# Kernel optimization log

Measured on AMD Instinct MI355X. Metric: run time of the kernel, lower is better.

Reference implementation:

```python
import jax, jax.numpy as jnp
import numpy as np
from jax.scipy.linalg import expm

U_SHAPE = (4, 32, 16, 16, 16, 3, 3)   # [mu, t, x, y, z, 3, 3]
W_SHAPE = (8, 32, 16, 16, 16, 3, 3)   # [feature, t, x, y, z, 3, 3]


def setup_inputs() -> dict:
    key = jax.random.key(0)
    k = jax.random.split(key, 5)
    return {
        "U_re": jax.random.normal(k[0], U_SHAPE, jnp.float32),
        "U_im": jax.random.normal(k[1], U_SHAPE, jnp.float32),
        "W_re": jax.random.normal(k[2], W_SHAPE, jnp.float32),
        "W_im": jax.random.normal(k[3], W_SHAPE, jnp.float32),
        "ah_weights": jax.random.normal(k[4], (4, W_SHAPE[0]), jnp.float32),
    }


def reference(U_re, U_im, W_re, W_im, ah_weights):
    U = (U_re + 1j * U_im).astype(jnp.complex64)
    W = (W_re + 1j * W_im).astype(jnp.complex64)

    # anti-hermitian part: W - W^dagger
    W_adj = jnp.conj(jnp.swapaxes(W, -1, -2))
    A = W - W_adj
    # traceless projection
    tr = jnp.trace(A, axis1=-2, axis2=-1)  # [i,t,x,y,z]
    A = A - (tr / 3.0)[..., None, None] * jnp.eye(3, dtype=A.dtype)

    # exponent: (1j*w) contracted with (-1j*A) == w contracted with A
    E = jnp.einsum('ui,itxyzab->utxyzab', ah_weights.astype(A.dtype), A)

    # batched 3x3 matrix exponential over the whole lattice
    E_flat = E.reshape(-1, 3, 3)
    expE = jax.vmap(expm)(E_flat).reshape(E.shape)

    # apply to gauge links: exp(...) @ U
    return jnp.einsum('utxyzij,utxyzjk->utxyzik', expE, U)
```

## Files before the change

### kernel.cpp

```cpp
#include <hip/hip_runtime.h>
#include <math.h>

#define NSITES 131072
#define PL     (NSITES * 9)

struct cplx { float re, im; };

__device__ __forceinline__ cplx cadd(cplx a, cplx b) { return {a.re + b.re, a.im + b.im}; }
__device__ __forceinline__ cplx cmul(cplx a, cplx b) {
    return { fmaf(a.re, b.re, -(a.im * b.im)), fmaf(a.re, b.im, a.im * b.re) };
}

struct __attribute__((aligned(4))) f3 { float x, y, z; };
__device__ __forceinline__ f3 ld3(const float* __restrict__ p) { return *(const f3*)p; }

struct Acc9 { float r01, r02, r12, i01, i02, i12, d0, d4, d8; };
struct Edof { float er01, er02, er12, ei01, ei02, ei12, ed0, ed1, ed2; };
struct G3   { cplx g0, g1, g2; };
struct C3   { cplx c0, c1, c2; };

__device__ __forceinline__ Edof make_edof(Acc9 a) {
    Edof E;
    E.er01 = a.r01; E.er02 = a.r02; E.er12 = a.r12;
    E.ei01 = a.i01; E.ei02 = a.i02; E.ei12 = a.i12;
    float t3 = (a.d0 + a.d4 + a.d8) * (2.f / 3.f);
    E.ed0 = fmaf(2.f, a.d0, -t3);
    E.ed1 = fmaf(2.f, a.d4, -t3);
    E.ed2 = fmaf(2.f, a.d8, -t3);
    return E;
}

__device__ __forceinline__ G3 expm_coeffs(Edof E)
{
    float r2 = fmaf(E.er01, E.er01, fmaf(E.er02, E.er02, fmaf(E.er12, E.er12,
               fmaf(E.ei01, E.ei01, fmaf(E.ei02, E.ei02, E.ei12 * E.ei12)))));
    r2 = fmaf(2.f, r2, fmaf(E.ed0, E.ed0, fmaf(E.ed1, E.ed1, E.ed2 * E.ed2)));

    const float n01 = fmaf(E.ei01, E.ei01, E.er01 * E.er01);
    const float n02 = fmaf(E.ei02, E.ei02, E.er02 * E.er02);
    const float n12 = fmaf(E.ei12, E.ei12, E.er12 * E.er12);
    const float zre = fmaf(E.ei01, E.ei12, -(E.er01 * E.er12));
    const float zim = -fmaf(E.ei01, E.er12, E.er01 * E.ei12);
    const float detH = E.ed0 * E.ed1 * E.ed2
                     + 2.f * fmaf(zre, E.ei02, -(zim * E.er02))
                     - fmaf(E.ed0, n12, fmaf(E.ed1, n02, E.ed2 * n01));

    int e; (void)frexpf(r2, &e);
    int sc = (e <= -2) ? 0 : min(1 + ((e + 1) >> 1), 40);
    const float inv  = __int_as_float((127 - sc) << 23);
    const float inv2 = inv * inv;
    const float px   = -0.5f * r2 * inv2;
    const float qxi  = -detH * (inv2 * inv);

    cplx T0 = {1.f, 0.f}, T1 = {0.f, 0.f}, T2 = {0.f, 0.f};
    cplx S0 = {1.f, 0.f}, S1 = {0.f, 0.f}, S2 = {0.f, 0.f};
    #pragma unroll
    for (int n = 1; n <= 10; n++) {
        float c  = 1.f / (float)n;
        float qc = qxi * c;
        cplx nT0 = { -qc * T2.im, qc * T2.re };
        cplx nT1 = { c * fmaf(px, T2.re, T0.re), c * fmaf(px, T2.im, T0.im) };
        cplx nT2 = { c * T1.re, c * T1.im };
        T0 = nT0; T1 = nT1; T2 = nT2;
        S0 = cadd(S0, T0); S1 = cadd(S1, T1); S2 = cadd(S2, T2);
    }

    const float q2 = 2.f * qxi;
    for (int k = 0; k < sc; k++) {
        cplx f0 = S0, f1 = S1, f2 = S2;
        cplx f12 = cmul(f1, f2);
        cplx f01 = cmul(f0, f1);
        cplx f02 = cmul(f0, f2);
        float f00re = fmaf(f0.re, f0.re, -(f0.im * f0.im)), f00im = 2.f * f0.re * f0.im;
        float f11re = fmaf(f1.re, f1.re, -(f1.im * f1.im)), f11im = 2.f * f1.re * f1.im;
        float f22re = fmaf(f2.re, f2.re, -(f2.im * f2.im)), f22im = 2.f * f2.re * f2.im;
        S0.re = fmaf(-q2, f12.im, f00re);
        S0.im = fmaf( q2, f12.re, f00im);
        S1.re = fmaf(-qxi, f22im, 2.f * fmaf(px, f12.re, f01.re));
        S1.im = fmaf( qxi, f22re, 2.f * fmaf(px, f12.im, f01.im));
        S2.re = fmaf(px, f22re, fmaf(2.f, f02.re, f11re));
        S2.im = fmaf(px, f22im, fmaf(2.f, f02.im, f11im));
    }
    G3 g;
    g.g0 = S0;
    g.g1 = { S1.re * inv,  S1.im * inv  };
    g.g2 = { S2.re * inv2, S2.im * inv2 };
    return g;
}

__device__ __forceinline__ C3 ecol(Edof E, C3 m)
{
    C3 v;
    v.c0.re = fmaf(-E.ed0, m.c0.im, fmaf(E.er01, m.c1.re, fmaf(-E.ei01, m.c1.im, fmaf(E.er02, m.c2.re, -(E.ei02 * m.c2.im)))));
    v.c0.im = fmaf( E.ed0, m.c0.re, fmaf(E.er01, m.c1.im, fmaf( E.ei01, m.c1.re, fmaf(E.er02, m.c2.im,  (E.ei02 * m.c2.re)))));
    v.c1.re = fmaf(-E.er01, m.c0.re, fmaf(-E.ei01, m.c0.im, fmaf(-E.ed1, m.c1.im, fmaf(E.er12, m.c2.re, -(E.ei12 * m.c2.im)))));
    v.c1.im = fmaf(-E.er01, m.c0.im, fmaf( E.ei01, m.c0.re, fmaf( E.ed1, m.c1.re, fmaf(E.er12, m.c2.im,  (E.ei12 * m.c2.re)))));
    v.c2.re = fmaf(-E.er02, m.c0.re, fmaf(-E.ei02, m.c0.im, fmaf(-E.er12, m.c1.re, fmaf(-E.ei12, m.c1.im, -(E.ed2 * m.c2.im)))));
    v.c2.im = fmaf(-E.er02, m.c0.im, fmaf( E.ei02, m.c0.re, fmaf(-E.er12, m.c1.im, fmaf( E.ei12, m.c1.re,  (E.ed2 * m.c2.re)))));
    return v;
}

__device__ __forceinline__ float ocomb(G3 g, cplx m, cplx v, cplx z) {
    return fmaf(g.g0.re, m.re, fmaf(-g.g0.im, m.im, fmaf(g.g1.re, v.re, fmaf(-g.g1.im, v.im,
           fmaf(g.g2.re, z.re, -(g.g2.im * z.im))))));
}

__device__ __forceinline__ void phase(Acc9 acc,
                                      const float* __restrict__ U_re,
                                      const float* __restrict__ U_im,
                                      float* __restrict__ out, size_t ub)
{
    f3 ua = ld3(U_re + ub), ubv = ld3(U_re + ub + 3), uc = ld3(U_re + ub + 6);
    f3 va = ld3(U_im + ub), vb  = ld3(U_im + ub + 3), vc = ld3(U_im + ub + 6);

    Edof E = make_edof(acc);
    G3 g = expm_coeffs(E);

    float o0,o1,o2,o3,o4,o5,o6,o7,o8;
    {
        C3 m = { cplx{ua.x, va.x}, cplx{ubv.x, vb.x}, cplx{uc.x, vc.x} };
        C3 v = ecol(E, m);
        C3 z = ecol(E, v);
        o0 = ocomb(g, m.c0, v.c0, z.c0);
        o3 = ocomb(g, m.c1, v.c1, z.c1);
        o6 = ocomb(g, m.c2, v.c2, z.c2);
    }
    {
        C3 m = { cplx{ua.y, va.y}, cplx{ubv.y, vb.y}, cplx{uc.y, vc.y} };
        C3 v = ecol(E, m);
        C3 z = ecol(E, v);
        o1 = ocomb(g, m.c0, v.c0, z.c0);
        o4 = ocomb(g, m.c1, v.c1, z.c1);
        o7 = ocomb(g, m.c2, v.c2, z.c2);
    }
    {
        C3 m = { cplx{ua.z, va.z}, cplx{ubv.z, vb.z}, cplx{uc.z, vc.z} };
        C3 v = ecol(E, m);
        C3 z = ecol(E, v);
        o2 = ocomb(g, m.c0, v.c0, z.c0);
        o5 = ocomb(g, m.c1, v.c1, z.c1);
        o8 = ocomb(g, m.c2, v.c2, z.c2);
    }
    float* ob = out + ub;
    *(f3*)(ob)     = { o0, o1, o2 };
    *(f3*)(ob + 3) = { o3, o4, o5 };
    *(f3*)(ob + 6) = { o6, o7, o8 };
}

__global__
__attribute__((amdgpu_flat_work_group_size(256, 256)))
__attribute__((amdgpu_waves_per_eu(4, 4)))
void lge_exp_kernel(
    const float* __restrict__ U_re, const float* __restrict__ U_im,
    const float* __restrict__ W_re, const float* __restrict__ W_im,
    const float* __restrict__ ahw,  float* __restrict__ out)
{
    const int gid  = blockIdx.x * 256 + threadIdx.x;
    const int site = gid >> 1;
    const int half = gid & 1;
    const size_t sb = (size_t)site * 9;

    Acc9 A0 = {0,0,0,0,0,0,0,0,0};
    Acc9 A1 = {0,0,0,0,0,0,0,0,0};

    #pragma unroll
    for (int f = 0; f < 8; f++) {
        const float* pr = W_re + (size_t)f * PL + sb;
        const float* pi = W_im + (size_t)f * PL + sb;
        f3 q  = ld3(pr + 1);
        f3 s  = ld3(pr + 5);
        f3 ia = ld3(pi), ib = ld3(pi + 3), ic = ld3(pi + 6);

        const float p0 = q.x - q.z;
        const float p1 = q.y - s.y;
        const float p2 = s.x - s.z;
        const float p3 = ia.y + ib.x;
        const float p4 = ia.z + ic.x;
        const float p5 = ib.z + ic.y;
        const float p6 = ia.x, p7 = ib.y, p8 = ic.z;

        const float wA = half ? ahw[1 * 8 + f] : ahw[0 * 8 + f];
        const float wB = half ? ahw[3 * 8 + f] : ahw[2 * 8 + f];

        A0.r01=fmaf(wA,p0,A0.r01); A0.r02=fmaf(wA,p1,A0.r02); A0.r12=fmaf(wA,p2,A0.r12);
        A0.i01=fmaf(wA,p3,A0.i01); A0.i02=fmaf(wA,p4,A0.i02); A0.i12=fmaf(wA,p5,A0.i12);
        A0.d0 =fmaf(wA,p6,A0.d0);  A0.d4 =fmaf(wA,p7,A0.d4);  A0.d8 =fmaf(wA,p8,A0.d8);

        A1.r01=fmaf(wB,p0,A1.r01); A1.r02=fmaf(wB,p1,A1.r02); A1.r12=fmaf(wB,p2,A1.r12);
        A1.i01=fmaf(wB,p3,A1.i01); A1.i02=fmaf(wB,p4,A1.i02); A1.i12=fmaf(wB,p5,A1.i12);
        A1.d0 =fmaf(wB,p6,A1.d0);  A1.d4 =fmaf(wB,p7,A1.d4);  A1.d8 =fmaf(wB,p8,A1.d8);
    }

    phase(A0, U_re, U_im, out, ((size_t)half * NSITES + site) * 9);
    __builtin_amdgcn_sched_barrier(0);
    phase(A1, U_re, U_im, out, ((size_t)(half + 2) * NSITES + site) * 9);
}

extern "C" void kernel_launch(void* const* d_in, const int* in_sizes, int n_in,
                              void* d_out, int out_size, void* d_ws, size_t ws_size,
                              hipStream_t stream) {
    const float* U_re = (const float*)d_in[0];
    const float* U_im = (const float*)d_in[1];
    const float* W_re = (const float*)d_in[2];
    const float* W_im = (const float*)d_in[3];
    const float* ahw  = (const float*)d_in[4];
    float* out = (float*)d_out;
    lge_exp_kernel<<<dim3(NSITES * 2 / 256), dim3(256), 0, stream>>>(
        U_re, U_im, W_re, W_im, ahw, out);
}
```

Before: 155.0 us.

## Map one thread per link direction instead of two per thread

Instead of each thread handling two directions of a site, each thread now handles one (site, mu) pair. The launch grid doubles and each thread recomputes the W accumulation for its own mu. The ahw weights are read as two float4 loads, and the W loads are batched four features at a time, with launch bounds changed to (256,2). This raises parallelism and lowers per-thread register pressure, at the cost of four threads per site redundantly loading the same W data. Those repeated loads should mostly hit cache, but they add load instructions and L1/L2 traffic.

```diff
diff --git a/kernel.cpp b/kernel.cpp
--- a/kernel.cpp
+++ b/kernel.cpp
@@ -13,11 +13,31 @@
 
 struct __attribute__((aligned(4))) f3 { float x, y, z; };
 __device__ __forceinline__ f3 ld3(const float* __restrict__ p) { return *(const f3*)p; }
+
+struct F5 { f3 q, s, ia, ib, ic; };
+__device__ __forceinline__ F5 ldw(const float* __restrict__ pr,
+                                  const float* __restrict__ pi) {
+    F5 r;
+    r.q  = ld3(pr + 1);
+    r.s  = ld3(pr + 5);
+    r.ia = ld3(pi);
+    r.ib = ld3(pi + 3);
+    r.ic = ld3(pi + 6);
+    return r;
+}
 
 struct Acc9 { float r01, r02, r12, i01, i02, i12, d0, d4, d8; };
 struct Edof { float er01, er02, er12, ei01, ei02, ei12, ed0, ed1, ed2; };
 struct G3   { cplx g0, g1, g2; };
 struct C3   { cplx c0, c1, c2; };
+
+#define ACCF(W, wf) do { \
+    const float p0 = W.q.x - W.q.z,  p1 = W.q.y - W.s.y,  p2 = W.s.x - W.s.z; \
+    const float p3 = W.ia.y + W.ib.x, p4 = W.ia.z + W.ic.x, p5 = W.ib.z + W.ic.y; \
+    A.r01 = fmaf(wf, p0, A.r01); A.r02 = fmaf(wf, p1, A.r02); A.r12 = fmaf(wf, p2, A.r12); \
+    A.i01 = fmaf(wf, p3, A.i01); A.i02 = fmaf(wf, p4, A.i02); A.i12 = fmaf(wf, p5, A.i12); \
+    A.d0  = fmaf(wf, W.ia.x, A.d0); A.d4 = fmaf(wf, W.ib.y, A.d4); A.d8 = fmaf(wf, W.ic.z, A.d8); \
+} while (0)
 
 __device__ __forceinline__ Edof make_edof(Acc9 a) {
     Edof E;
@@ -105,16 +125,42 @@
            fmaf(g.g2.re, z.re, -(g.g2.im * z.im))))));
 }
 
-__device__ __forceinline__ void phase(Acc9 acc,
-                                      const float* __restrict__ U_re,
-                                      const float* __restrict__ U_im,
-                                      float* __restrict__ out, size_t ub)
+__global__ __launch_bounds__(256, 2) void lge_exp_kernel(
+    const float* __restrict__ U_re, const float* __restrict__ U_im,
+    const float* __restrict__ W_re, const float* __restrict__ W_im,
+    const float* __restrict__ ahw,  float* __restrict__ out)
 {
+    const int gid   = blockIdx.x * 256 + threadIdx.x;
+    const int gsite = gid >> 2;
+    const int mu    = gid & 3;
+    const size_t sb = (size_t)gsite * 9;
+
+    const size_t ub = ((size_t)mu * NSITES + gsite) * 9;
     f3 ua = ld3(U_re + ub), ubv = ld3(U_re + ub + 3), uc = ld3(U_re + ub + 6);
     f3 va = ld3(U_im + ub), vb  = ld3(U_im + ub + 3), vc = ld3(U_im + ub + 6);
 
-    Edof E = make_edof(acc);
-    G3 g = expm_coeffs(E);
+    const float4* ahw4 = (const float4*)ahw;
+    float4 wlo = ahw4[mu * 2], whi = ahw4[mu * 2 + 1];
+
+    Acc9 A = {0,0,0,0,0,0,0,0,0};
+
+    {
+        F5 w0 = ldw(W_re + (size_t)0 * PL + sb, W_im + (size_t)0 * PL + sb);
+        F5 w1 = ldw(W_re + (size_t)1 * PL + sb, W_im + (size_t)1 * PL + sb);
+        F5 w2 = ldw(W_re + (size_t)2 * PL + sb, W_im + (size_t)2 * PL + sb);
+        F5 w3 = ldw(W_re + (size_t)3 * PL + sb, W_im + (size_t)3 * PL + sb);
+        ACCF(w0, wlo.x); ACCF(w1, wlo.y); ACCF(w2, wlo.z); ACCF(w3, wlo.w);
+    }
+    {
+        F5 w4 = ldw(W_re + (size_t)4 * PL + sb, W_im + (size_t)4 * PL + sb);
+        F5 w5 = ldw(W_re + (size_t)5 * PL + sb, W_im + (size_t)5 * PL + sb);
+        F5 w6 = ldw(W_re + (size_t)6 * PL + sb, W_im + (size_t)6 * PL + sb);
+        F5 w7 = ldw(W_re + (size_t)7 * PL + sb, W_im + (size_t)7 * PL + sb);
+        ACCF(w4, whi.x); ACCF(w5, whi.y); ACCF(w6, whi.z); ACCF(w7, whi.w);
+    }
+
+    const Edof E = make_edof(A);
+    const G3 g = expm_coeffs(E);
 
     float o0,o1,o2,o3,o4,o5,o6,o7,o8;
     {
@@ -145,55 +191,6 @@
     *(f3*)(ob)     = { o0, o1, o2 };
     *(f3*)(ob + 3) = { o3, o4, o5 };
     *(f3*)(ob + 6) = { o6, o7, o8 };
-}
-
-__global__
-__attribute__((amdgpu_flat_work_group_size(256, 256)))
-__attribute__((amdgpu_waves_per_eu(4, 4)))
-void lge_exp_kernel(
-    const float* __restrict__ U_re, const float* __restrict__ U_im,
-    const float* __restrict__ W_re, const float* __restrict__ W_im,
-    const float* __restrict__ ahw,  float* __restrict__ out)
-{
-    const int gid  = blockIdx.x * 256 + threadIdx.x;
-    const int site = gid >> 1;
-    const int half = gid & 1;
-    const size_t sb = (size_t)site * 9;
-
-    Acc9 A0 = {0,0,0,0,0,0,0,0,0};
-    Acc9 A1 = {0,0,0,0,0,0,0,0,0};
-
-    #pragma unroll
-    for (int f = 0; f < 8; f++) {
-        const float* pr = W_re + (size_t)f * PL + sb;
-        const float* pi = W_im + (size_t)f * PL + sb;
-        f3 q  = ld3(pr + 1);
-        f3 s  = ld3(pr + 5);
-        f3 ia = ld3(pi), ib = ld3(pi + 3), ic = ld3(pi + 6);
-
-        const float p0 = q.x - q.z;
-        const float p1 = q.y - s.y;
-        const float p2 = s.x - s.z;
-        const float p3 = ia.y + ib.x;
-        const float p4 = ia.z + ic.x;
-        const float p5 = ib.z + ic.y;
-        const float p6 = ia.x, p7 = ib.y, p8 = ic.z;
-
-        const float wA = half ? ahw[1 * 8 + f] : ahw[0 * 8 + f];
-        const float wB = half ? ahw[3 * 8 + f] : ahw[2 * 8 + f];
-
-        A0.r01=fmaf(wA,p0,A0.r01); A0.r02=fmaf(wA,p1,A0.r02); A0.r12=fmaf(wA,p2,A0.r12);
-        A0.i01=fmaf(wA,p3,A0.i01); A0.i02=fmaf(wA,p4,A0.i02); A0.i12=fmaf(wA,p5,A0.i12);
-        A0.d0 =fmaf(wA,p6,A0.d0);  A0.d4 =fmaf(wA,p7,A0.d4);  A0.d8 =fmaf(wA,p8,A0.d8);
-
-        A1.r01=fmaf(wB,p0,A1.r01); A1.r02=fmaf(wB,p1,A1.r02); A1.r12=fmaf(wB,p2,A1.r12);
-        A1.i01=fmaf(wB,p3,A1.i01); A1.i02=fmaf(wB,p4,A1.i02); A1.i12=fmaf(wB,p5,A1.i12);
-        A1.d0 =fmaf(wB,p6,A1.d0);  A1.d4 =fmaf(wB,p7,A1.d4);  A1.d8 =fmaf(wB,p8,A1.d8);
-    }
-
-    phase(A0, U_re, U_im, out, ((size_t)half * NSITES + site) * 9);
-    __builtin_amdgcn_sched_barrier(0);
-    phase(A1, U_re, U_im, out, ((size_t)(half + 2) * NSITES + site) * 9);
 }
 
 extern "C" void kernel_launch(void* const* d_in, const int* in_sizes, int n_in,
@@ -205,6 +202,6 @@
     const float* W_im = (const float*)d_in[3];
     const float* ahw  = (const float*)d_in[4];
     float* out = (float*)d_out;
-    lge_exp_kernel<<<dim3(NSITES * 2 / 256), dim3(256), 0, stream>>>(
+    lge_exp_kernel<<<dim3(NSITES * 4 / 256), dim3(256), 0, stream>>>(
         U_re, U_im, W_re, W_im, ahw, out);
 }
```

Result: faster. 145.7 us (-6.0%).
